# Performance work log

Measured on AMD Instinct MI355X. Metric: run time of the kernel, lower is better.

The kernel has to match this reference:

```python
import jax, jax.numpy as jnp
import numpy as np

B, T, D, E, P = 4, 2048, 1024, 8, 1024

def setup_inputs() -> dict:
    key = jax.random.key(0)
    k1, k2, k3 = jax.random.split(key, 3)
    x = jax.random.normal(k1, (B, T, D), dtype=jnp.float32)
    gate_w = jax.random.normal(k2, (D, E), dtype=jnp.float32) * (1.0 / np.sqrt(D))
    gate_b = jnp.zeros((E,), dtype=jnp.float32)
    expert_w = jax.random.normal(k3, (E, D, P), dtype=jnp.float32) * (1.0 / np.sqrt(D))
    expert_b = jnp.zeros((E, P), dtype=jnp.float32)
    return {"x": x, "gate_w": gate_w, "gate_b": gate_b,
            "expert_w": expert_w, "expert_b": expert_b}

def reference(x, gate_w, gate_b, expert_w, expert_b):
    # gating: Dense(E) with softmax -> [B, T, E]
    gate = jax.nn.softmax(jnp.einsum('btd,de->bte', x, gate_w) + gate_b, axis=-1)
    # all experts as one batched GEMM: [B, T, E, P]
    expert_out = jnp.einsum('btd,edp->btep', x, expert_w) + expert_b
    # gate-weighted sum over experts -> [B, T, P]
    out = jnp.einsum('bte,btep->btp', gate, expert_out)
    return out
```

## Files before the change

kernel.cpp:

```cpp
#include <hip/hip_runtime.h>
#include <hip/hip_bf16.h>
#include <math.h>

#define M_TOT 8192
#define D_DIM 1024
#define E_NUM 8
#define P_DIM 1024
#define K_TOT (E_NUM * D_DIM)

typedef __attribute__((ext_vector_type(8))) short short8;
typedef __attribute__((ext_vector_type(4))) float f32x4;
typedef __attribute__((ext_vector_type(8))) unsigned short u16x8;

static __device__ __forceinline__ unsigned short f2bf(float f) {
  unsigned u = __builtin_bit_cast(unsigned, f);
  unsigned r = (u + 0x7fffu + ((u >> 16) & 1u)) >> 16;
  return (unsigned short)r;
}

__global__ __launch_bounds__(256) void gate_kernel(const float* __restrict__ x,
                                                   const float* __restrict__ gw,
                                                   const float* __restrict__ gb,
                                                   float* __restrict__ gate) {
  const int row  = blockIdx.x * 4 + (threadIdx.x >> 6);
  const int lane = threadIdx.x & 63;
  const float* xr = x + (size_t)row * D_DIM;
  float acc[E_NUM];
#pragma unroll
  for (int e = 0; e < E_NUM; ++e) acc[e] = 0.f;
#pragma unroll
  for (int it = 0; it < 16; ++it) {
    const int d = it * 64 + lane;
    const float xv = xr[d];
    const float4* g4 = reinterpret_cast<const float4*>(gw + (size_t)d * E_NUM);
    float4 a = g4[0], b = g4[1];
    acc[0] += xv * a.x; acc[1] += xv * a.y; acc[2] += xv * a.z; acc[3] += xv * a.w;
    acc[4] += xv * b.x; acc[5] += xv * b.y; acc[6] += xv * b.z; acc[7] += xv * b.w;
  }
#pragma unroll
  for (int off = 32; off >= 1; off >>= 1) {
#pragma unroll
    for (int e = 0; e < E_NUM; ++e) acc[e] += __shfl_xor(acc[e], off, 64);
  }
  if (lane == 0) {
    float v[E_NUM], mx = -1e30f;
#pragma unroll
    for (int e = 0; e < E_NUM; ++e) { v[e] = acc[e] + gb[e]; mx = fmaxf(mx, v[e]); }
    float s = 0.f;
#pragma unroll
    for (int e = 0; e < E_NUM; ++e) { v[e] = expf(v[e] - mx); s += v[e]; }
    const float inv = 1.f / s;
#pragma unroll
    for (int e = 0; e < E_NUM; ++e) gate[(size_t)row * E_NUM + e] = v[e] * inv;
  }
}

__global__ __launch_bounds__(256) void wtrans2_kernel(const float* __restrict__ w,
                                                      unsigned short* __restrict__ wt) {
  __shared__ float tile[64][65];
  const int e  = blockIdx.z;
  const int p0 = blockIdx.y * 64;
  const int d0 = blockIdx.x * 64;
  const int tx = threadIdx.x & 63;
  const int ty = threadIdx.x >> 6;
  const float* src = w + ((size_t)e * D_DIM + d0) * P_DIM + p0;
#pragma unroll
  for (int i = 0; i < 16; ++i) {
    const int dr = i * 4 + ty;
    tile[dr][tx] = src[(size_t)dr * P_DIM + tx];
  }
  __syncthreads();
#pragma unroll
  for (int i = 0; i < 16; ++i) {
    const int pr = i * 4 + ty;
    const int c = tx ^ ((pr & 7) << 3);
    wt[(size_t)(p0 + pr) * K_TOT + e * D_DIM + d0 + c] = f2bf(tile[tx][pr]);
  }
}

__global__ __launch_bounds__(256) void aprep_kernel(const float* __restrict__ x,
                                                    const float* __restrict__ gate,
                                                    unsigned short* __restrict__ ap) {
  const int tid = threadIdx.x;
  const int m   = blockIdx.x * 2 + (tid >> 7);
  const int jd  = tid & 127;
  const float4* xp = reinterpret_cast<const float4*>(x + (size_t)m * D_DIM + jd * 8);
  const float4 p = xp[0], q = xp[1];
  unsigned short* row = ap + (size_t)m * K_TOT;
  const int cbase = (jd >> 3) * 8 + ((jd & 7) ^ (m & 7));
#pragma unroll
  for (int e = 0; e < E_NUM; ++e) {
    const float gs = gate[(size_t)m * E_NUM + e];
    u16x8 v;
    v[0] = f2bf(p.x * gs); v[1] = f2bf(p.y * gs);
    v[2] = f2bf(p.z * gs); v[3] = f2bf(p.w * gs);
    v[4] = f2bf(q.x * gs); v[5] = f2bf(q.y * gs);
    v[6] = f2bf(q.z * gs); v[7] = f2bf(q.w * gs);
    *reinterpret_cast<u16x8*>(&row[(size_t)(e * 128 + cbase) * 8]) = v;
  }
}

static __device__ __forceinline__ short8 ldfrag(const unsigned short* buf, int row, int e0) {
  return *reinterpret_cast<const short8*>(&buf[row * 64 + (e0 ^ ((row & 7) << 3))]);
}

__global__ __launch_bounds__(512, 1) void gemm_sk_kernel(
    const unsigned short* __restrict__ ap,
    const unsigned short* __restrict__ wt,
    const float* __restrict__ gate,
    const float* __restrict__ eb,
    float* __restrict__ out) {
  __shared__ __align__(16) unsigned short lA[2 * 2 * 8192];
  __shared__ __align__(16) unsigned short lB[2 * 2 * 8192];
  __shared__ float lG[256 * 8];

  const int tid  = threadIdx.x;
  const int lane = tid & 63;
  const int wid  = tid >> 6;
  const int wm   = wid >> 2;
  const int wn   = wid & 3;
  const int l15  = lane & 15;
  const int e0b  = (lane >> 4) * 8;

  const int bid = blockIdx.x;
  const int c   = bid & 7, j = bid >> 3;
  const int kh  = j & 1;
  const int nt  = (j >> 1) & 3;
  const int mt  = c * 4 + (j >> 3);
  const int m0  = mt * 256, n0 = nt * 256;
  const int kb  = kh * 64;

  reinterpret_cast<float4*>(lG)[tid] =
      reinterpret_cast<const float4*>(gate + (size_t)m0 * E_NUM)[tid];
  __syncthreads();

  auto stA = [&](int tt, int h) {
    const int w = kb + (tt & 63), b = tt & 1;
#pragma unroll
    for (int l = 0; l < 2; ++l) {
      const int u = tid + l * 512;
      const unsigned short* src =
          ap + (size_t)(m0 + h * 128 + (u >> 3)) * K_TOT + w * 64 + (u & 7) * 8;
      __builtin_amdgcn_global_load_lds(
          (const __attribute__((address_space(1))) void*)src,
          (__attribute__((address_space(3))) void*)&lA[(b * 2 + h) * 8192 + u * 8], 16, 0, 0);
    }
  };
  auto stB = [&](int tt, int h) {
    const int w = kb + (tt & 63), b = tt & 1;
#pragma unroll
    for (int l = 0; l < 2; ++l) {
      const int u = tid + l * 512;
      const unsigned short* src =
          wt + (size_t)(n0 + h * 128 + (u >> 3)) * K_TOT + w * 64 + (u & 7) * 8;
      __builtin_amdgcn_global_load_lds(
          (const __attribute__((address_space(1))) void*)src,
          (__attribute__((address_space(3))) void*)&lB[(b * 2 + h) * 8192 + u * 8], 16, 0, 0);
    }
  };

  f32x4 acc[8][4];
#pragma unroll
  for (int i = 0; i < 8; ++i)
#pragma unroll
    for (int jj = 0; jj < 4; ++jj)
#pragma unroll
      for (int k = 0; k < 4; ++k) acc[i][jj][k] = 0.f;

  stB(0, 0); stB(0, 1); stA(0, 0); stA(0, 1);
  stB(1, 0); stB(1, 1);
  asm volatile("s_waitcnt vmcnt(4)" ::: "memory");
  __builtin_amdgcn_s_barrier();
  asm volatile("" ::: "memory");

  const int rbB = (wn & 1) * 64;
  const int hB  = wn >> 1;

#pragma unroll 2
  for (int t = 0; t < 64; ++t) {
    const int b = t & 1;
    const unsigned short* bufA = lA + (b * 2 + wm) * 8192;
    const unsigned short* bufB = lB + (b * 2 + hB) * 8192;

    short8 a0[4][2], a1[4][2], b0[2][2], b1[2][2];

#pragma unroll
    for (int mi = 0; mi < 4; ++mi)
#pragma unroll
      for (int kk = 0; kk < 2; ++kk)
        a0[mi][kk] = ldfrag(bufA, mi * 16 + l15, kk * 32 + e0b);
#pragma unroll
    for (int ni = 0; ni < 2; ++ni)
#pragma unroll
      for (int kk = 0; kk < 2; ++kk)
        b0[ni][kk] = ldfrag(bufB, rbB + ni * 16 + l15, kk * 32 + e0b);
    stA(t + 1, 0);
    __builtin_amdgcn_s_barrier();
    asm volatile("s_waitcnt lgkmcnt(0)" ::: "memory");
    __builtin_amdgcn_s_setprio(1);
#pragma unroll
    for (int mi = 0; mi < 4; ++mi)
#pragma unroll
      for (int ni = 0; ni < 2; ++ni)
#pragma unroll
        for (int kk = 0; kk < 2; ++kk)
          acc[mi][ni] = __builtin_amdgcn_mfma_f32_16x16x32_bf16(a0[mi][kk], b0[ni][kk], acc[mi][ni], 0, 0, 0);
    __builtin_amdgcn_s_setprio(0);
    __builtin_amdgcn_s_barrier();
    asm volatile("" ::: "memory");

#pragma unroll
    for (int ni = 0; ni < 2; ++ni)
#pragma unroll
      for (int kk = 0; kk < 2; ++kk)
        b1[ni][kk] = ldfrag(bufB, rbB + 32 + ni * 16 + l15, kk * 32 + e0b);
    stA(t + 1, 1);
    __builtin_amdgcn_s_barrier();
    asm volatile("s_waitcnt lgkmcnt(0)" ::: "memory");
    __builtin_amdgcn_s_setprio(1);
#pragma unroll
    for (int mi = 0; mi < 4; ++mi)
#pragma unroll
      for (int ni = 0; ni < 2; ++ni)
#pragma unroll
        for (int kk = 0; kk < 2; ++kk)
          acc[mi][2 + ni] = __builtin_amdgcn_mfma_f32_16x16x32_bf16(a0[mi][kk], b1[ni][kk], acc[mi][2 + ni], 0, 0, 0);
    __builtin_amdgcn_s_setprio(0);
    __builtin_amdgcn_s_barrier();
    asm volatile("" ::: "memory");

#pragma unroll
    for (int mi = 0; mi < 4; ++mi)
#pragma unroll
      for (int kk = 0; kk < 2; ++kk)
        a1[mi][kk] = ldfrag(bufA, 64 + mi * 16 + l15, kk * 32 + e0b);
    stB(t + 2, 0);
    __builtin_amdgcn_s_barrier();
    asm volatile("s_waitcnt lgkmcnt(0)" ::: "memory");
    __builtin_amdgcn_s_setprio(1);
#pragma unroll
    for (int mi = 0; mi < 4; ++mi)
#pragma unroll
      for (int ni = 0; ni < 2; ++ni)
#pragma unroll
        for (int kk = 0; kk < 2; ++kk)
          acc[4 + mi][ni] = __builtin_amdgcn_mfma_f32_16x16x32_bf16(a1[mi][kk], b0[ni][kk], acc[4 + mi][ni], 0, 0, 0);
    __builtin_amdgcn_s_setprio(0);
    __builtin_amdgcn_s_barrier();
    asm volatile("" ::: "memory");

    stB(t + 2, 1);
    __builtin_amdgcn_s_setprio(1);
#pragma unroll
    for (int mi = 0; mi < 4; ++mi)
#pragma unroll
      for (int ni = 0; ni < 2; ++ni)
#pragma unroll
        for (int kk = 0; kk < 2; ++kk)
          acc[4 + mi][2 + ni] = __builtin_amdgcn_mfma_f32_16x16x32_bf16(a1[mi][kk], b1[ni][kk], acc[4 + mi][2 + ni], 0, 0, 0);
    __builtin_amdgcn_s_setprio(0);
    asm volatile("s_waitcnt vmcnt(4)" ::: "memory");
    __builtin_amdgcn_s_barrier();
    asm volatile("" ::: "memory");
  }

#pragma unroll
  for (int nf = 0; nf < 4; ++nf) {
    const int C = n0 + wn * 64 + nf * 16 + l15;
    float lb[E_NUM];
    if (kh == 0) {
#pragma unroll
      for (int e = 0; e < E_NUM; ++e) lb[e] = eb[(size_t)e * P_DIM + C];
    }
#pragma unroll
    for (int mf = 0; mf < 8; ++mf) {
#pragma unroll
      for (int reg = 0; reg < 4; ++reg) {
        const int rl = wm * 128 + mf * 16 + (lane >> 4) * 4 + reg;
        float v = acc[mf][nf][reg];
        if (kh == 0) {
          float bs = 0.f;
#pragma unroll
          for (int e = 0; e < E_NUM; ++e) bs += lG[rl * 8 + e] * lb[e];
          v += bs;
        }
        atomicAdd(&out[(size_t)(m0 + rl) * P_DIM + C], v);
      }
    }
  }
}


__global__ __launch_bounds__(256) void wtrans_kernel(const float* __restrict__ w,
                                                     unsigned short* __restrict__ wt) {
  __shared__ float tile[64][65];
  const int e  = blockIdx.z;
  const int p0 = blockIdx.y * 64;
  const int d0 = blockIdx.x * 64;
  const int tx = threadIdx.x & 63;
  const int ty = threadIdx.x >> 6;
  const float* src = w + ((size_t)e * D_DIM + d0) * P_DIM + p0;
#pragma unroll
  for (int i = 0; i < 16; ++i) {
    const int dr = i * 4 + ty;
    tile[dr][tx] = src[(size_t)dr * P_DIM + tx];
  }
  __syncthreads();
  unsigned short* dst = wt + ((size_t)e * P_DIM + p0) * D_DIM + d0;
#pragma unroll
  for (int i = 0; i < 16; ++i) {
    const int pr = i * 4 + ty;
    const int cc = tx ^ ((pr & 7) << 3);
    dst[(size_t)pr * D_DIM + cc] = f2bf(tile[tx][pr]);
  }
}

__global__ __launch_bounds__(256, 2) void moe_gemm_kernel(
    const float* __restrict__ x,
    const unsigned short* __restrict__ wt,
    const float* __restrict__ gate,
    const float* __restrict__ eb,
    float* __restrict__ out) {
  __shared__ unsigned short lA[128 * 64];
  __shared__ unsigned short lB[128 * 64];
  __shared__ float lG[128 * 8];
  __shared__ float lBias[E_NUM * 128];

  const int tid  = threadIdx.x;
  const int lane = tid & 63;
  const int wid  = tid >> 6;
  const int wr   = wid >> 1, wc = wid & 1;
  const int m0   = blockIdx.x * 128;
  const int n0   = blockIdx.y * 128;

  reinterpret_cast<float4*>(lG)[tid] =
      reinterpret_cast<const float4*>(gate + (size_t)m0 * E_NUM)[tid];
  {
    const int e = tid >> 5, cc = (tid & 31) * 4;
    *reinterpret_cast<float4*>(&lBias[e * 128 + cc]) =
        *reinterpret_cast<const float4*>(&eb[(size_t)e * P_DIM + n0 + cc]);
  }
  __syncthreads();

  const int rA   = tid >> 1;
  const int colA = (tid & 1) * 32;
  const float* xrow = x + (size_t)(m0 + rA) * D_DIM + colA;

  f32x4 acc[4][4];
#pragma unroll
  for (int i = 0; i < 4; ++i)
#pragma unroll
    for (int jj = 0; jj < 4; ++jj)
#pragma unroll
      for (int k = 0; k < 4; ++k) acc[i][jj][k] = 0.f;

  for (int e = 0; e < E_NUM; ++e) {
    const float gs = lG[rA * 8 + e];
    const unsigned short* wte = wt + ((size_t)e * P_DIM + n0) * D_DIM;
    for (int kt = 0; kt < 16; ++kt) {
      __syncthreads();
      const float4* apv = reinterpret_cast<const float4*>(xrow + kt * 64);
#pragma unroll
      for (int jj = 0; jj < 4; ++jj) {
        float4 p = apv[2 * jj], q = apv[2 * jj + 1];
        u16x8 v;
        v[0] = f2bf(p.x * gs); v[1] = f2bf(p.y * gs);
        v[2] = f2bf(p.z * gs); v[3] = f2bf(p.w * gs);
        v[4] = f2bf(q.x * gs); v[5] = f2bf(q.y * gs);
        v[6] = f2bf(q.z * gs); v[7] = f2bf(q.w * gs);
        const int idx = rA * 64 + ((colA + jj * 8) ^ ((rA & 7) << 3));
        *reinterpret_cast<u16x8*>(&lA[idx]) = v;
      }
#pragma unroll
      for (int i = 0; i < 4; ++i) {
        const int u  = tid + i * 256;
        const int rr = u >> 3;
        const int cc = u & 7;
        const unsigned short* src = wte + (size_t)rr * D_DIM + kt * 64 + cc * 8;
        __builtin_amdgcn_global_load_lds(
            (const __attribute__((address_space(1))) void*)src,
            (__attribute__((address_space(3))) void*)&lB[u * 8], 16, 0, 0);
      }
      __syncthreads();
#pragma unroll
      for (int kk = 0; kk < 2; ++kk) {
        const int e0 = kk * 32 + (lane >> 4) * 8;
        short8 a[4], b[4];
#pragma unroll
        for (int m = 0; m < 4; ++m) {
          const int r = wr * 64 + m * 16 + (lane & 15);
          a[m] = *reinterpret_cast<const short8*>(&lA[r * 64 + (e0 ^ ((r & 7) << 3))]);
        }
#pragma unroll
        for (int n = 0; n < 4; ++n) {
          const int r = wc * 64 + n * 16 + (lane & 15);
          b[n] = *reinterpret_cast<const short8*>(&lB[r * 64 + (e0 ^ ((r & 7) << 3))]);
        }
#pragma unroll
        for (int m = 0; m < 4; ++m)
#pragma unroll
          for (int n = 0; n < 4; ++n)
            acc[m][n] = __builtin_amdgcn_mfma_f32_16x16x32_bf16(a[m], b[n], acc[m][n], 0, 0, 0);
      }
    }
  }

#pragma unroll
  for (int m = 0; m < 4; ++m) {
#pragma unroll
    for (int n = 0; n < 4; ++n) {
      const int rbase = wr * 64 + m * 16 + ((lane >> 4) * 4);
      const int cl    = wc * 64 + n * 16 + (lane & 15);
#pragma unroll
      for (int reg = 0; reg < 4; ++reg) {
        const int r = rbase + reg;
        float bsum = 0.f;
#pragma unroll
        for (int e = 0; e < E_NUM; ++e) bsum += lG[r * 8 + e] * lBias[e * 128 + cl];
        out[(size_t)(m0 + r) * P_DIM + n0 + cl] = acc[m][n][reg] + bsum;
      }
    }
  }
}


extern "C" void kernel_launch(void* const* d_in, const int* in_sizes, int n_in,
                              void* d_out, int out_size, void* d_ws, size_t ws_size,
                              hipStream_t stream) {
  const float* x  = (const float*)d_in[0];
  const float* gw = (const float*)d_in[1];
  const float* gb = (const float*)d_in[2];
  const float* ew = (const float*)d_in[3];
  const float* eb = (const float*)d_in[4];
  float* out = (float*)d_out;

  char* ws = (char*)d_ws;
  float* gate        = (float*)ws;
  unsigned short* wt = (unsigned short*)(ws + 262144);

  const size_t need_big = 262144ull + 16777216ull + 134217728ull;

  gate_kernel<<<M_TOT / 4, 256, 0, stream>>>(x, gw, gb, gate);

  if (ws_size >= need_big) {
    unsigned short* apb = (unsigned short*)(ws + 262144 + 16777216);
    hipMemsetAsync(d_out, 0, (size_t)out_size * sizeof(float), stream);
    wtrans2_kernel<<<dim3(D_DIM / 64, P_DIM / 64, E_NUM), 256, 0, stream>>>(ew, wt);
    aprep_kernel<<<M_TOT / 2, 256, 0, stream>>>(x, gate, apb);
    gemm_sk_kernel<<<256, 512, 0, stream>>>(apb, wt, gate, eb, out);
  } else {
    wtrans_kernel<<<dim3(D_DIM / 64, P_DIM / 64, E_NUM), 256, 0, stream>>>(ew, wt);
    moe_gemm_kernel<<<dim3(M_TOT / 128, P_DIM / 128), 256, 0, stream>>>(x, wt, gate, eb, out);
  }
}
```

Measured before the change: 232.8 us.

## Restructure GEMM to 4-stage K=32 pipeline with one barrier per step

```diff
diff --git a/kernel.cpp b/kernel.cpp
--- a/kernel.cpp
+++ b/kernel.cpp
@@ -73,8 +73,11 @@
 #pragma unroll
   for (int i = 0; i < 16; ++i) {
     const int pr = i * 4 + ty;
-    const int c = tx ^ ((pr & 7) << 3);
-    wt[(size_t)(p0 + pr) * K_TOT + e * D_DIM + d0 + c] = f2bf(tile[tx][pr]);
+    const int blk = e * 32 + (d0 >> 5) + (tx >> 5);
+    const int c   = (tx >> 3) & 3;
+    const int j   = tx & 7;
+    const int cs  = c ^ ((pr >> 1) & 3);
+    wt[(size_t)(p0 + pr) * K_TOT + blk * 32 + cs * 8 + j] = f2bf(tile[tx][pr]);
   }
 }
 
@@ -87,7 +90,8 @@
   const float4* xp = reinterpret_cast<const float4*>(x + (size_t)m * D_DIM + jd * 8);
   const float4 p = xp[0], q = xp[1];
   unsigned short* row = ap + (size_t)m * K_TOT;
-  const int cbase = (jd >> 3) * 8 + ((jd & 7) ^ (m & 7));
+  const int blk0 = jd >> 2;
+  const int cs   = (jd & 3) ^ ((m >> 1) & 3);
 #pragma unroll
   for (int e = 0; e < E_NUM; ++e) {
     const float gs = gate[(size_t)m * E_NUM + e];
@@ -96,22 +100,18 @@
     v[2] = f2bf(p.z * gs); v[3] = f2bf(p.w * gs);
     v[4] = f2bf(q.x * gs); v[5] = f2bf(q.y * gs);
     v[6] = f2bf(q.z * gs); v[7] = f2bf(q.w * gs);
-    *reinterpret_cast<u16x8*>(&row[(size_t)(e * 128 + cbase) * 8]) = v;
-  }
-}
-
-static __device__ __forceinline__ short8 ldfrag(const unsigned short* buf, int row, int e0) {
-  return *reinterpret_cast<const short8*>(&buf[row * 64 + (e0 ^ ((row & 7) << 3))]);
-}
-
-__global__ __launch_bounds__(512, 1) void gemm_sk_kernel(
+    *reinterpret_cast<u16x8*>(&row[(size_t)(e * 32 + blk0) * 32 + cs * 8]) = v;
+  }
+}
+
+__global__ __launch_bounds__(512, 1) void gemm_q_kernel(
     const unsigned short* __restrict__ ap,
     const unsigned short* __restrict__ wt,
     const float* __restrict__ gate,
     const float* __restrict__ eb,
     float* __restrict__ out) {
-  __shared__ __align__(16) unsigned short lA[2 * 2 * 8192];
-  __shared__ __align__(16) unsigned short lB[2 * 2 * 8192];
+  __shared__ __align__(16) unsigned short lA[4 * 8192];
+  __shared__ __align__(16) unsigned short lB[4 * 8192];
   __shared__ float lG[256 * 8];
 
   const int tid  = threadIdx.x;
@@ -120,7 +120,7 @@
   const int wm   = wid >> 2;
   const int wn   = wid & 3;
   const int l15  = lane & 15;
-  const int e0b  = (lane >> 4) * 8;
+  const int g8   = (lane >> 4);
 
   const int bid = blockIdx.x;
   const int c   = bid & 7, j = bid >> 3;
@@ -128,36 +128,31 @@
   const int nt  = (j >> 1) & 3;
   const int mt  = c * 4 + (j >> 3);
   const int m0  = mt * 256, n0 = nt * 256;
-  const int kb  = kh * 64;
+  const int kb  = kh * 128;
 
   reinterpret_cast<float4*>(lG)[tid] =
       reinterpret_cast<const float4*>(gate + (size_t)m0 * E_NUM)[tid];
-  __syncthreads();
-
-  auto stA = [&](int tt, int h) {
-    const int w = kb + (tt & 63), b = tt & 1;
-#pragma unroll
-    for (int l = 0; l < 2; ++l) {
-      const int u = tid + l * 512;
-      const unsigned short* src =
-          ap + (size_t)(m0 + h * 128 + (u >> 3)) * K_TOT + w * 64 + (u & 7) * 8;
-      __builtin_amdgcn_global_load_lds(
-          (const __attribute__((address_space(1))) void*)src,
-          (__attribute__((address_space(3))) void*)&lA[(b * 2 + h) * 8192 + u * 8], 16, 0, 0);
-    }
+
+  const unsigned short* aB0 = ap + (size_t)(m0 + (tid >> 2)) * K_TOT + (tid & 3) * 8;
+  const unsigned short* bB0 = wt + (size_t)(n0 + (tid >> 2)) * K_TOT + (tid & 3) * 8;
+
+  auto stage = [&](int t) {
+    const int w = kb + (t & 127);
+    const int b = t & 3;
+    const size_t wo = (size_t)w * 32;
+    __builtin_amdgcn_global_load_lds(
+        (const __attribute__((address_space(1))) void*)(aB0 + wo),
+        (__attribute__((address_space(3))) void*)&lA[b * 8192 + tid * 8], 16, 0, 0);
+    __builtin_amdgcn_global_load_lds(
+        (const __attribute__((address_space(1))) void*)(aB0 + (size_t)128 * K_TOT + wo),
+        (__attribute__((address_space(3))) void*)&lA[b * 8192 + (tid + 512) * 8], 16, 0, 0);
+    __builtin_amdgcn_global_load_lds(
+        (const __attribute__((address_space(1))) void*)(bB0 + wo),
+        (__attribute__((address_space(3))) void*)&lB[b * 8192 + tid * 8], 16, 0, 0);
+    __builtin_amdgcn_global_load_lds(
+        (const __attribute__((address_space(1))) void*)(bB0 + (size_t)128 * K_TOT + wo),
+        (__attribute__((address_space(3))) void*)&lB[b * 8192 + (tid + 512) * 8], 16, 0, 0);
   };
-  auto stB = [&](int tt, int h) {
-    const int w = kb + (tt & 63), b = tt & 1;
-#pragma unroll
-    for (int l = 0; l < 2; ++l) {
-      const int u = tid + l * 512;
-      const unsigned short* src =
-          wt + (size_t)(n0 + h * 128 + (u >> 3)) * K_TOT + w * 64 + (u & 7) * 8;
-      __builtin_amdgcn_global_load_lds(
-          (const __attribute__((address_space(1))) void*)src,
-          (__attribute__((address_space(3))) void*)&lB[(b * 2 + h) * 8192 + u * 8], 16, 0, 0);
-    }
-  };
 
   f32x4 acc[8][4];
 #pragma unroll
@@ -167,99 +162,41 @@
 #pragma unroll
       for (int k = 0; k < 4; ++k) acc[i][jj][k] = 0.f;
 
-  stB(0, 0); stB(0, 1); stA(0, 0); stA(0, 1);
-  stB(1, 0); stB(1, 1);
-  asm volatile("s_waitcnt vmcnt(4)" ::: "memory");
+  stage(0); stage(1); stage(2);
+  asm volatile("s_waitcnt vmcnt(8) lgkmcnt(0)" ::: "memory");
   __builtin_amdgcn_s_barrier();
   asm volatile("" ::: "memory");
 
-  const int rbB = (wn & 1) * 64;
-  const int hB  = wn >> 1;
-
-#pragma unroll 2
-  for (int t = 0; t < 64; ++t) {
-    const int b = t & 1;
-    const unsigned short* bufA = lA + (b * 2 + wm) * 8192;
-    const unsigned short* bufB = lB + (b * 2 + hB) * 8192;
-
-    short8 a0[4][2], a1[4][2], b0[2][2], b1[2][2];
-
-#pragma unroll
-    for (int mi = 0; mi < 4; ++mi)
-#pragma unroll
-      for (int kk = 0; kk < 2; ++kk)
-        a0[mi][kk] = ldfrag(bufA, mi * 16 + l15, kk * 32 + e0b);
-#pragma unroll
-    for (int ni = 0; ni < 2; ++ni)
-#pragma unroll
-      for (int kk = 0; kk < 2; ++kk)
-        b0[ni][kk] = ldfrag(bufB, rbB + ni * 16 + l15, kk * 32 + e0b);
-    stA(t + 1, 0);
-    __builtin_amdgcn_s_barrier();
+#pragma unroll 1
+  for (int t = 0; t < 128; ++t) {
+    const int b = t & 3;
+    const unsigned short* bufA = lA + b * 8192;
+    const unsigned short* bufB = lB + b * 8192;
+
+    stage(t + 3);
+
+    short8 a[8], bfr[4];
+#pragma unroll
+    for (int mi = 0; mi < 8; ++mi) {
+      const int r = wm * 128 + mi * 16 + l15;
+      a[mi] = *reinterpret_cast<const short8*>(&bufA[r * 32 + ((g8 ^ ((r >> 1) & 3)) << 3)]);
+    }
+#pragma unroll
+    for (int ni = 0; ni < 4; ++ni) {
+      const int r = wn * 64 + ni * 16 + l15;
+      bfr[ni] = *reinterpret_cast<const short8*>(&bufB[r * 32 + ((g8 ^ ((r >> 1) & 3)) << 3)]);
+    }
+
+    __builtin_amdgcn_s_setprio(1);
+#pragma unroll
+    for (int mi = 0; mi < 8; ++mi)
+#pragma unroll
+      for (int ni = 0; ni < 4; ++ni)
+        acc[mi][ni] = __builtin_amdgcn_mfma_f32_16x16x32_bf16(a[mi], bfr[ni], acc[mi][ni], 0, 0, 0);
+    __builtin_amdgcn_s_setprio(0);
+
     asm volatile("s_waitcnt lgkmcnt(0)" ::: "memory");
-    __builtin_amdgcn_s_setprio(1);
-#pragma unroll
-    for (int mi = 0; mi < 4; ++mi)
-#pragma unroll
-      for (int ni = 0; ni < 2; ++ni)
-#pragma unroll
-        for (int kk = 0; kk < 2; ++kk)
-          acc[mi][ni] = __builtin_amdgcn_mfma_f32_16x16x32_bf16(a0[mi][kk], b0[ni][kk], acc[mi][ni], 0, 0, 0);
-    __builtin_amdgcn_s_setprio(0);
-    __builtin_amdgcn_s_barrier();
-    asm volatile("" ::: "memory");
-
-#pragma unroll
-    for (int ni = 0; ni < 2; ++ni)
-#pragma unroll
-      for (int kk = 0; kk < 2; ++kk)
-        b1[ni][kk] = ldfrag(bufB, rbB + 32 + ni * 16 + l15, kk * 32 + e0b);
-    stA(t + 1, 1);
-    __builtin_amdgcn_s_barrier();
-    asm volatile("s_waitcnt lgkmcnt(0)" ::: "memory");
-    __builtin_amdgcn_s_setprio(1);
-#pragma unroll
-    for (int mi = 0; mi < 4; ++mi)
-#pragma unroll
-      for (int ni = 0; ni < 2; ++ni)
-#pragma unroll
-        for (int kk = 0; kk < 2; ++kk)
-          acc[mi][2 + ni] = __builtin_amdgcn_mfma_f32_16x16x32_bf16(a0[mi][kk], b1[ni][kk], acc[mi][2 + ni], 0, 0, 0);
-    __builtin_amdgcn_s_setprio(0);
-    __builtin_amdgcn_s_barrier();
-    asm volatile("" ::: "memory");
-
-#pragma unroll
-    for (int mi = 0; mi < 4; ++mi)
-#pragma unroll
-      for (int kk = 0; kk < 2; ++kk)
-        a1[mi][kk] = ldfrag(bufA, 64 + mi * 16 + l15, kk * 32 + e0b);
-    stB(t + 2, 0);
-    __builtin_amdgcn_s_barrier();
-    asm volatile("s_waitcnt lgkmcnt(0)" ::: "memory");
-    __builtin_amdgcn_s_setprio(1);
-#pragma unroll
-    for (int mi = 0; mi < 4; ++mi)
-#pragma unroll
-      for (int ni = 0; ni < 2; ++ni)
-#pragma unroll
-        for (int kk = 0; kk < 2; ++kk)
-          acc[4 + mi][ni] = __builtin_amdgcn_mfma_f32_16x16x32_bf16(a1[mi][kk], b0[ni][kk], acc[4 + mi][ni], 0, 0, 0);
-    __builtin_amdgcn_s_setprio(0);
-    __builtin_amdgcn_s_barrier();
-    asm volatile("" ::: "memory");
-
-    stB(t + 2, 1);
-    __builtin_amdgcn_s_setprio(1);
-#pragma unroll
-    for (int mi = 0; mi < 4; ++mi)
-#pragma unroll
-      for (int ni = 0; ni < 2; ++ni)
-#pragma unroll
-        for (int kk = 0; kk < 2; ++kk)
-          acc[4 + mi][2 + ni] = __builtin_amdgcn_mfma_f32_16x16x32_bf16(a1[mi][kk], b1[ni][kk], acc[4 + mi][2 + ni], 0, 0, 0);
-    __builtin_amdgcn_s_setprio(0);
-    asm volatile("s_waitcnt vmcnt(4)" ::: "memory");
+    asm volatile("s_waitcnt vmcnt(8)" ::: "memory");
     __builtin_amdgcn_s_barrier();
     asm volatile("" ::: "memory");
   }
@@ -447,7 +384,7 @@
     hipMemsetAsync(d_out, 0, (size_t)out_size * sizeof(float), stream);
     wtrans2_kernel<<<dim3(D_DIM / 64, P_DIM / 64, E_NUM), 256, 0, stream>>>(ew, wt);
     aprep_kernel<<<M_TOT / 2, 256, 0, stream>>>(x, gate, apb);
-    gemm_sk_kernel<<<256, 512, 0, stream>>>(apb, wt, gate, eb, out);
+    gemm_q_kernel<<<256, 512, 0, stream>>>(apb, wt, gate, eb, out);
   } else {
     wtrans_kernel<<<dim3(D_DIM / 64, P_DIM / 64, E_NUM), 256, 0, stream>>>(ew, wt);
     moe_gemm_kernel<<<dim3(M_TOT / 128, P_DIM / 128), 256, 0, stream>>>(x, wt, gate, eb, out);
```

Result: slower. 245.6 us (+5.5%).
